# Kernel optimization log

Measured on AMD Instinct MI355X. Metric: run time of the kernel, lower is better.

## Reference

```python
import jax, jax.numpy as jnp
import numpy as np

NUM_ORI = 8      # num_orientations
P = 7            # pooled height/width (out_size)
S = 2            # num_samples (sampling grid per bin side)
SCALE = 0.25     # spatial_scale
CLOCKWISE = False


def setup_inputs() -> dict:
    key = jax.random.key(0)
    kf, kb, kc, ks, ka = jax.random.split(key, 5)
    B, C, H, W = 2, 256, 256, 256   # C = 32 channel groups x 8 orientations
    R = 512
    features = jax.random.normal(kf, (B, C, H, W), dtype=jnp.float32)
    img = H / SCALE                 # image-space extent (1024)
    batch_idx = jax.random.randint(kb, (R,), 0, B).astype(jnp.float32)
    ctr = jax.random.uniform(kc, (R, 2), minval=0.0, maxval=img)
    wh = jax.random.uniform(ks, (R, 2), minval=32.0, maxval=img * 0.25)
    ang = jax.random.uniform(ka, (R,), minval=-np.pi, maxval=np.pi)
    rois = jnp.concatenate([batch_idx[:, None], ctr, wh, ang[:, None]], axis=1)
    return {"features": features, "rois": rois}


def _riroi_align_rotated(features, rois):
    B, C, H, W = features.shape
    O = NUM_ORI
    Cg = C // O
    R = rois.shape[0]
    f32 = features.dtype

    b = rois[:, 0].astype(jnp.int32)
    cx = rois[:, 1] * SCALE
    cy = rois[:, 2] * SCALE
    rw = jnp.maximum(rois[:, 3] * SCALE, 1.0)
    rh = jnp.maximum(rois[:, 4] * SCALE, 1.0)
    theta = rois[:, 5]

    # --- orientation channel alignment (uses original-sign theta) ---
    ind_f = theta * O / (2.0 * np.pi)
    ind_floor = jnp.floor(ind_f)
    l_var = ind_f - ind_floor                         # (R,)
    r_var = 1.0 - l_var
    ind = jnp.mod(ind_floor.astype(jnp.int32), O)     # start channel, (R,)
    o = jnp.arange(O)
    ind_rot = jnp.mod(o[None, :] - ind[:, None], O)   # (R,O)
    ind_rot_p = jnp.mod(ind_rot + 1, O)

    if CLOCKWISE:
        theta = -theta

    # --- rotated sampling grid, (R, Ph, Pw, Sy, Sx) ---
    bin_h = rh / P
    bin_w = rw / P
    pidx = jnp.arange(P, dtype=f32)
    sidx = jnp.arange(S, dtype=f32)
    yy = (-rh[:, None, None] / 2.0 + pidx[None, :, None] * bin_h[:, None, None]
          + (sidx[None, None, :] + 0.5) * bin_h[:, None, None] / S)   # (R,Ph,Sy)
    xx = (-rw[:, None, None] / 2.0 + pidx[None, :, None] * bin_w[:, None, None]
          + (sidx[None, None, :] + 0.5) * bin_w[:, None, None] / S)   # (R,Pw,Sx)
    ct = jnp.cos(theta)[:, None, None, None, None]
    st = jnp.sin(theta)[:, None, None, None, None]
    X = xx[:, None, :, None, :]   # (R,1,Pw,1,Sx)
    Y = yy[:, :, None, :, None]   # (R,Ph,1,Sy,1)
    x = (X * ct - Y * st + cx[:, None, None, None, None]).reshape(R, -1)  # (R,K)
    y = (X * st + Y * ct + cy[:, None, None, None, None]).reshape(R, -1)

    # --- bilinear interpolation (matches mmcv bilinear_interpolate) ---
    valid = ~((y < -1.0) | (y > H) | (x < -1.0) | (x > W))
    yc = jnp.clip(y, 0.0, None)
    xc = jnp.clip(x, 0.0, None)
    y0 = yc.astype(jnp.int32)
    x0 = xc.astype(jnp.int32)
    hi_y = y0 >= H - 1
    hi_x = x0 >= W - 1
    y1 = jnp.where(hi_y, H - 1, y0 + 1)
    y0 = jnp.where(hi_y, H - 1, y0)
    yc = jnp.where(hi_y, y0.astype(f32), yc)
    x1 = jnp.where(hi_x, W - 1, x0 + 1)
    x0 = jnp.where(hi_x, W - 1, x0)
    xc = jnp.where(hi_x, x0.astype(f32), xc)
    ly = yc - y0.astype(f32); hy = 1.0 - ly
    lx = xc - x0.astype(f32); hx = 1.0 - lx
    vf = valid.astype(f32)
    w1 = (hy * hx * vf)[..., None]
    w2 = (hy * lx * vf)[..., None]
    w3 = (ly * hx * vf)[..., None]
    w4 = (ly * lx * vf)[..., None]

    bb = b[:, None]                                     # (R,1) -> broadcast (R,K)
    v = (w1 * features[bb, :, y0, x0] + w2 * features[bb, :, y0, x1]
         + w3 * features[bb, :, y1, x0] + w4 * features[bb, :, y1, x1])  # (R,K,C)

    # average over the SxS sample grid per bin
    v = v.reshape(R, P, P, S, S, Cg, O).mean(axis=(3, 4))   # (R,P,P,Cg,O)

    # orientation channel cyclic blend
    idx = ind_rot[:, None, None, None, :]               # (R,1,1,1,O)
    idx_p = ind_rot_p[:, None, None, None, :]
    rb = r_var[:, None, None, None, None]
    lb = l_var[:, None, None, None, None]
    out = rb * jnp.take_along_axis(v, idx, axis=4) + lb * jnp.take_along_axis(v, idx_p, axis=4)
    # (R,Ph,Pw,Cg,O) -> (R, Cg, O, Ph, Pw) -> (R, C, Ph, Pw)
    return out.transpose(0, 3, 4, 1, 2).reshape(R, Cg * O, P, P)


def reference(features, rois):
    return _riroi_align_rotated(features, rois)
```

## Files before the change

kernel.cpp:

```cpp
#include <hip/hip_runtime.h>


#define NORI 8
#define PBIN 7
#define NSAMP 2
#define CCH 256
#define HH 256
#define WW 256
#define PTOT (HH * WW)

__global__ __launch_bounds__(256) void nchw_to_nhwc_kernel(
    const float* __restrict__ feat, float* __restrict__ nhwc)
{
    __shared__ float tile[16][260];
    const int t  = threadIdx.x;
    const int b  = blockIdx.x / (PTOT / 16);
    const int p0 = (blockIdx.x % (PTOT / 16)) * 16;

    const int pl4 = (t & 3) * 4;
    const int cl  = t >> 2;
    #pragma unroll
    for (int k = 0; k < 4; ++k) {
        const int c = cl + 64 * k;
        const float4 v = *reinterpret_cast<const float4*>(
            feat + ((size_t)b * CCH + c) * PTOT + p0 + pl4);
        tile[pl4 + 0][c] = v.x;
        tile[pl4 + 1][c] = v.y;
        tile[pl4 + 2][c] = v.z;
        tile[pl4 + 3][c] = v.w;
    }
    __syncthreads();

    const int c4 = (t & 63) * 4;
    const int plb = t >> 6;
    #pragma unroll
    for (int k = 0; k < 4; ++k) {
        const int pl = plb + 4 * k;
        float4 v;
        v.x = tile[pl][c4 + 0];
        v.y = tile[pl][c4 + 1];
        v.z = tile[pl][c4 + 2];
        v.w = tile[pl][c4 + 3];
        *reinterpret_cast<float4*>(
            nhwc + ((size_t)b * PTOT + p0 + pl) * CCH + c4) = v;
    }
}

__global__ __launch_bounds__(256) void riroi_gather_nhwc_kernel(
    const float* __restrict__ nhwc,
    const float* __restrict__ rois,
    float* __restrict__ out)
{
    __shared__ float stage[64 * 49];

    const int r  = blockIdx.x >> 2;
    const int q  = blockIdx.x & 3;
    const int t  = threadIdx.x;
    const int cl = t & 63;
    const int c  = q * 64 + cl;
    const int o  = c & (NORI - 1);
    const int pix_base = t >> 6;

    const float* roi = rois + r * 6;
    const int   b     = (int)roi[0];
    const float cx    = roi[1] * 0.25f;
    const float cy    = roi[2] * 0.25f;
    const float rw    = fmaxf(roi[3] * 0.25f, 1.0f);
    const float rh    = fmaxf(roi[4] * 0.25f, 1.0f);
    const float theta = roi[5];

    const float ind_f     = theta * (8.0f / 6.283185307179586f);
    const float ind_floor = floorf(ind_f);
    const float l_var     = ind_f - ind_floor;
    const float r_var     = 1.0f - l_var;
    const int   ind       = (((int)ind_floor % NORI) + NORI) % NORI;

    const float bin_h = rh * (1.0f / (float)PBIN);
    const float bin_w = rw * (1.0f / (float)PBIN);
    const float ct = cosf(theta);
    const float st = sinf(theta);
    const float Hf = (float)HH, Wf = (float)WW;

    const float* __restrict__ fb = nhwc + (size_t)b * PTOT * CCH;

    const int lane = t & 63;
    const int lbase = lane & ~(NORI - 1);
    const int osrc  = (o - ind + NORI) & (NORI - 1);
    const int osrc1 = (osrc + 1) & (NORI - 1);

    for (int pix = pix_base; pix < PBIN * PBIN; pix += 4) {
        const int ph = pix / PBIN;
        const int pw = pix - ph * PBIN;
        const float y_base = -rh * 0.5f + (float)ph * bin_h;
        const float x_base = -rw * 0.5f + (float)pw * bin_w;

        float acc = 0.0f;
        #pragma unroll
        for (int sy = 0; sy < NSAMP; ++sy) {
            #pragma unroll
            for (int sx = 0; sx < NSAMP; ++sx) {
                const float Y = y_base + ((float)sy + 0.5f) * bin_h * 0.5f;
                const float X = x_base + ((float)sx + 0.5f) * bin_w * 0.5f;
                const float x = X * ct - Y * st + cx;
                const float y = X * st + Y * ct + cy;

                const bool valid = !((y < -1.0f) || (y > Hf) || (x < -1.0f) || (x > Wf));
                float yc = fmaxf(y, 0.0f);
                float xc = fmaxf(x, 0.0f);
                int y0 = (int)yc;
                int x0 = (int)xc;
                int y1, x1;
                if (y0 >= HH - 1) { y0 = HH - 1; y1 = HH - 1; yc = (float)y0; }
                else              { y1 = y0 + 1; }
                if (x0 >= WW - 1) { x0 = WW - 1; x1 = WW - 1; xc = (float)x0; }
                else              { x1 = x0 + 1; }

                const float ly = yc - (float)y0, hy = 1.0f - ly;
                const float lx = xc - (float)x0, hx = 1.0f - lx;
                const float vf = valid ? 1.0f : 0.0f;
                const float w1 = hy * hx * vf;
                const float w2 = hy * lx * vf;
                const float w3 = ly * hx * vf;
                const float w4 = ly * lx * vf;

                const float f00 = fb[((size_t)y0 * WW + x0) * CCH + c];
                const float f01 = fb[((size_t)y0 * WW + x1) * CCH + c];
                const float f10 = fb[((size_t)y1 * WW + x0) * CCH + c];
                const float f11 = fb[((size_t)y1 * WW + x1) * CCH + c];
                acc += w1 * f00 + w2 * f01 + w3 * f10 + w4 * f11;
            }
        }
        const float v = acc * 0.25f;

        const float v0 = __shfl(v, lbase | osrc,  64);
        const float v1 = __shfl(v, lbase | osrc1, 64);
        stage[cl * 49 + pix] = r_var * v0 + l_var * v1;
    }
    __syncthreads();

    float* __restrict__ dst = out + (size_t)r * (CCH * PBIN * PBIN) + q * (64 * PBIN * PBIN);
    #pragma unroll
    for (int k = 0; k < 13; ++k) {
        const int i = t + 256 * k;
        if (i < 64 * 49) dst[i] = stage[i];
    }
}

__global__ __launch_bounds__(256) void riroi_align_rotated_kernel(
    const float* __restrict__ feat, const float* __restrict__ rois,
    float* __restrict__ out, int C, int H, int W)
{
    const int blk = blockIdx.x;
    const int r   = blk / (PBIN * PBIN);
    const int pix = blk % (PBIN * PBIN);
    const int ph  = pix / PBIN;
    const int pw  = pix % PBIN;
    const int c   = threadIdx.x;
    const int o   = c & (NORI - 1);

    const float* roi = rois + r * 6;
    const int   b     = (int)roi[0];
    const float cx    = roi[1] * 0.25f;
    const float cy    = roi[2] * 0.25f;
    const float rw    = fmaxf(roi[3] * 0.25f, 1.0f);
    const float rh    = fmaxf(roi[4] * 0.25f, 1.0f);
    const float theta = roi[5];

    const float ind_f     = theta * (8.0f / 6.283185307179586f);
    const float ind_floor = floorf(ind_f);
    const float l_var     = ind_f - ind_floor;
    const float r_var     = 1.0f - l_var;
    const int ind = (((int)ind_floor % NORI) + NORI) % NORI;

    const float bin_h = rw * 0.0f + rh * (1.0f / (float)PBIN);
    const float bin_w = rw * (1.0f / (float)PBIN);
    const float ct = cosf(theta);
    const float st = sinf(theta);

    const float* __restrict__ fbc = feat + ((size_t)b * C + c) * (size_t)(H * W);
    const float Hf = (float)H, Wf = (float)W;
    const float y_base = -rh * 0.5f + (float)ph * bin_h;
    const float x_base = -rw * 0.5f + (float)pw * bin_w;

    float acc = 0.0f;
    #pragma unroll
    for (int sy = 0; sy < NSAMP; ++sy) {
        #pragma unroll
        for (int sx = 0; sx < NSAMP; ++sx) {
            const float Y = y_base + ((float)sy + 0.5f) * bin_h * 0.5f;
            const float X = x_base + ((float)sx + 0.5f) * bin_w * 0.5f;
            float x = X * ct - Y * st + cx;
            float y = X * st + Y * ct + cy;
            const bool valid = !((y < -1.0f) || (y > Hf) || (x < -1.0f) || (x > Wf));
            float yc = fmaxf(y, 0.0f);
            float xc = fmaxf(x, 0.0f);
            int y0 = (int)yc;
            int x0 = (int)xc;
            int y1, x1;
            if (y0 >= H - 1) { y0 = H - 1; y1 = H - 1; yc = (float)y0; }
            else             { y1 = y0 + 1; }
            if (x0 >= W - 1) { x0 = W - 1; x1 = W - 1; xc = (float)x0; }
            else             { x1 = x0 + 1; }
            const float ly = yc - (float)y0, hy = 1.0f - ly;
            const float lx = xc - (float)x0, hx = 1.0f - lx;
            const float vf = valid ? 1.0f : 0.0f;
            const float w1 = hy * hx * vf, w2 = hy * lx * vf;
            const float w3 = ly * hx * vf, w4 = ly * lx * vf;
            acc += w1 * fbc[y0 * W + x0] + w2 * fbc[y0 * W + x1]
                 + w3 * fbc[y1 * W + x0] + w4 * fbc[y1 * W + x1];
        }
    }
    const float v = acc * 0.25f;
    const int lane  = threadIdx.x & 63;
    const int base  = lane & ~(NORI - 1);
    const int osrc  = (o - ind + NORI) & (NORI - 1);
    const float v0 = __shfl(v, base | osrc, 64);
    const float v1 = __shfl(v, base | ((osrc + 1) & (NORI - 1)), 64);
    out[((size_t)r * C + c) * (PBIN * PBIN) + ph * PBIN + pw] = r_var * v0 + l_var * v1;
}

extern "C" void kernel_launch(void* const* d_in, const int* in_sizes, int n_in,
                              void* d_out, int out_size, void* d_ws, size_t ws_size,
                              hipStream_t stream) {
    const float* feat = (const float*)d_in[0];
    const float* rois = (const float*)d_in[1];
    float* out = (float*)d_out;

    const int R = in_sizes[1] / 6;
    const int B = in_sizes[0] / (CCH * PTOT);
    const size_t need = (size_t)B * PTOT * CCH * sizeof(float);

    if (ws_size >= need) {
        float* nhwc = (float*)d_ws;
        nchw_to_nhwc_kernel<<<dim3(B * (PTOT / 16)), dim3(256), 0, stream>>>(feat, nhwc);
        riroi_gather_nhwc_kernel<<<dim3(R * 4), dim3(256), 0, stream>>>(nhwc, rois, out);
    } else {
        riroi_align_rotated_kernel<<<dim3(R * PBIN * PBIN), dim3(256), 0, stream>>>(
            feat, rois, out, CCH, HH, WW);
    }
}
```

Measured before the change: 279.2 us.

## Retile NHWC transpose and vectorize gather with float4 channel loads

The transpose kernel now handles 32 pixels by 128 channels per block and issues all global loads before the shared-memory writes, which gives more loads in flight. The gather kernel has each thread load four adjacent channels with float4 reads and process four pixels in an unrolled loop. The orientation blend moves from wavefront shuffles to the shared-memory write-back stage, where it costs extra LDS reads and integer index math. This trades fewer, wider memory transactions and more memory parallelism against more per-thread registers and possible LDS bank conflicts.

```diff
diff --git a/kernel.cpp b/kernel.cpp
--- a/kernel.cpp
+++ b/kernel.cpp
@@ -3,7 +3,7 @@
 
 #define NORI 8
 #define PBIN 7
-#define NSAMP 2
+#define NPIX 49
 #define CCH 256
 #define HH 256
 #define WW 256
@@ -12,37 +12,48 @@
 __global__ __launch_bounds__(256) void nchw_to_nhwc_kernel(
     const float* __restrict__ feat, float* __restrict__ nhwc)
 {
-    __shared__ float tile[16][260];
-    const int t  = threadIdx.x;
-    const int b  = blockIdx.x / (PTOT / 16);
-    const int p0 = (blockIdx.x % (PTOT / 16)) * 16;
-
-    const int pl4 = (t & 3) * 4;
-    const int cl  = t >> 2;
-    #pragma unroll
-    for (int k = 0; k < 4; ++k) {
-        const int c = cl + 64 * k;
-        const float4 v = *reinterpret_cast<const float4*>(
-            feat + ((size_t)b * CCH + c) * PTOT + p0 + pl4);
-        tile[pl4 + 0][c] = v.x;
-        tile[pl4 + 1][c] = v.y;
-        tile[pl4 + 2][c] = v.z;
-        tile[pl4 + 3][c] = v.w;
+    __shared__ float tile[32 * 132];
+    const int t = threadIdx.x;
+    int blk = blockIdx.x;
+    const int b    = blk >> 12;
+    blk &= 4095;
+    const int c0   = (blk & 1) * 128;
+    const int p0   = (blk >> 1) * 32;
+
+    const float* __restrict__ src = feat + ((size_t)b * CCH + c0) * PTOT + p0;
+
+    float4 v[4];
+    #pragma unroll
+    for (int k = 0; k < 4; ++k) {
+        const int flat = t + 256 * k;
+        const int c    = flat >> 3;
+        const int p4   = (flat & 7) * 4;
+        v[k] = *reinterpret_cast<const float4*>(src + (size_t)c * PTOT + p4);
+    }
+    #pragma unroll
+    for (int k = 0; k < 4; ++k) {
+        const int flat = t + 256 * k;
+        const int c    = flat >> 3;
+        const int p4   = (flat & 7) * 4;
+        tile[(p4 + 0) * 132 + c] = v[k].x;
+        tile[(p4 + 1) * 132 + c] = v[k].y;
+        tile[(p4 + 2) * 132 + c] = v[k].z;
+        tile[(p4 + 3) * 132 + c] = v[k].w;
     }
     __syncthreads();
 
-    const int c4 = (t & 63) * 4;
-    const int plb = t >> 6;
-    #pragma unroll
-    for (int k = 0; k < 4; ++k) {
-        const int pl = plb + 4 * k;
-        float4 v;
-        v.x = tile[pl][c4 + 0];
-        v.y = tile[pl][c4 + 1];
-        v.z = tile[pl][c4 + 2];
-        v.w = tile[pl][c4 + 3];
-        *reinterpret_cast<float4*>(
-            nhwc + ((size_t)b * PTOT + p0 + pl) * CCH + c4) = v;
+    float* __restrict__ dst = nhwc + ((size_t)b * PTOT + p0) * CCH + c0;
+    #pragma unroll
+    for (int k = 0; k < 4; ++k) {
+        const int flat = t + 256 * k;
+        const int p    = flat >> 5;
+        const int cg4  = (flat & 31) * 4;
+        float4 w;
+        w.x = tile[p * 132 + cg4 + 0];
+        w.y = tile[p * 132 + cg4 + 1];
+        w.z = tile[p * 132 + cg4 + 2];
+        w.w = tile[p * 132 + cg4 + 3];
+        *reinterpret_cast<float4*>(dst + (size_t)p * CCH + cg4) = w;
     }
 }
 
@@ -51,15 +62,14 @@
     const float* __restrict__ rois,
     float* __restrict__ out)
 {
-    __shared__ float stage[64 * 49];
-
-    const int r  = blockIdx.x >> 2;
-    const int q  = blockIdx.x & 3;
-    const int t  = threadIdx.x;
-    const int cl = t & 63;
-    const int c  = q * 64 + cl;
-    const int o  = c & (NORI - 1);
-    const int pix_base = t >> 6;
+    __shared__ float stage[64 * NPIX];
+
+    const int r   = blockIdx.x >> 2;
+    const int q   = blockIdx.x & 3;
+    const int t   = threadIdx.x;
+    const int cl4 = (t & 15) * 4;
+    const int c4  = q * 64 + cl4;
+    const int pixlane = t >> 4;
 
     const float* roi = rois + r * 6;
     const int   b     = (int)roi[0];
@@ -83,66 +93,79 @@
 
     const float* __restrict__ fb = nhwc + (size_t)b * PTOT * CCH;
 
-    const int lane = t & 63;
-    const int lbase = lane & ~(NORI - 1);
-    const int osrc  = (o - ind + NORI) & (NORI - 1);
-    const int osrc1 = (osrc + 1) & (NORI - 1);
-
-    for (int pix = pix_base; pix < PBIN * PBIN; pix += 4) {
-        const int ph = pix / PBIN;
-        const int pw = pix - ph * PBIN;
-        const float y_base = -rh * 0.5f + (float)ph * bin_h;
-        const float x_base = -rw * 0.5f + (float)pw * bin_w;
-
-        float acc = 0.0f;
-        #pragma unroll
-        for (int sy = 0; sy < NSAMP; ++sy) {
+    #pragma unroll
+    for (int k = 0; k < 4; ++k) {
+        const int pix = pixlane + 16 * k;
+        if (pix < NPIX) {
+            const int ph = pix / PBIN;
+            const int pw = pix - ph * PBIN;
+            const float y_base = -rh * 0.5f + (float)ph * bin_h;
+            const float x_base = -rw * 0.5f + (float)pw * bin_w;
+
+            float ax = 0.0f, ay = 0.0f, az = 0.0f, aw = 0.0f;
             #pragma unroll
-            for (int sx = 0; sx < NSAMP; ++sx) {
-                const float Y = y_base + ((float)sy + 0.5f) * bin_h * 0.5f;
-                const float X = x_base + ((float)sx + 0.5f) * bin_w * 0.5f;
-                const float x = X * ct - Y * st + cx;
-                const float y = X * st + Y * ct + cy;
-
-                const bool valid = !((y < -1.0f) || (y > Hf) || (x < -1.0f) || (x > Wf));
-                float yc = fmaxf(y, 0.0f);
-                float xc = fmaxf(x, 0.0f);
-                int y0 = (int)yc;
-                int x0 = (int)xc;
-                int y1, x1;
-                if (y0 >= HH - 1) { y0 = HH - 1; y1 = HH - 1; yc = (float)y0; }
-                else              { y1 = y0 + 1; }
-                if (x0 >= WW - 1) { x0 = WW - 1; x1 = WW - 1; xc = (float)x0; }
-                else              { x1 = x0 + 1; }
-
-                const float ly = yc - (float)y0, hy = 1.0f - ly;
-                const float lx = xc - (float)x0, hx = 1.0f - lx;
-                const float vf = valid ? 1.0f : 0.0f;
-                const float w1 = hy * hx * vf;
-                const float w2 = hy * lx * vf;
-                const float w3 = ly * hx * vf;
-                const float w4 = ly * lx * vf;
-
-                const float f00 = fb[((size_t)y0 * WW + x0) * CCH + c];
-                const float f01 = fb[((size_t)y0 * WW + x1) * CCH + c];
-                const float f10 = fb[((size_t)y1 * WW + x0) * CCH + c];
-                const float f11 = fb[((size_t)y1 * WW + x1) * CCH + c];
-                acc += w1 * f00 + w2 * f01 + w3 * f10 + w4 * f11;
+            for (int sy = 0; sy < 2; ++sy) {
+                #pragma unroll
+                for (int sx = 0; sx < 2; ++sx) {
+                    const float Y = y_base + ((float)sy + 0.5f) * bin_h * 0.5f;
+                    const float X = x_base + ((float)sx + 0.5f) * bin_w * 0.5f;
+                    const float x = X * ct - Y * st + cx;
+                    const float y = X * st + Y * ct + cy;
+
+                    const bool valid = !((y < -1.0f) || (y > Hf) || (x < -1.0f) || (x > Wf));
+                    float yc = fmaxf(y, 0.0f);
+                    float xc = fmaxf(x, 0.0f);
+                    int y0 = (int)yc;
+                    int x0 = (int)xc;
+                    int y1, x1;
+                    if (y0 >= HH - 1) { y0 = HH - 1; y1 = HH - 1; yc = (float)y0; }
+                    else              { y1 = y0 + 1; }
+                    if (x0 >= WW - 1) { x0 = WW - 1; x1 = WW - 1; xc = (float)x0; }
+                    else              { x1 = x0 + 1; }
+
+                    const float ly = yc - (float)y0, hy = 1.0f - ly;
+                    const float lx = xc - (float)x0, hx = 1.0f - lx;
+                    const float vf = valid ? 1.0f : 0.0f;
+                    const float w1 = hy * hx * vf;
+                    const float w2 = hy * lx * vf;
+                    const float w3 = ly * hx * vf;
+                    const float w4 = ly * lx * vf;
+
+                    const float4 f00 = *reinterpret_cast<const float4*>(
+                        fb + ((size_t)(y0 * WW + x0)) * CCH + c4);
+                    const float4 f01 = *reinterpret_cast<const float4*>(
+                        fb + ((size_t)(y0 * WW + x1)) * CCH + c4);
+                    const float4 f10 = *reinterpret_cast<const float4*>(
+                        fb + ((size_t)(y1 * WW + x0)) * CCH + c4);
+                    const float4 f11 = *reinterpret_cast<const float4*>(
+                        fb + ((size_t)(y1 * WW + x1)) * CCH + c4);
+
+                    ax += w1 * f00.x + w2 * f01.x + w3 * f10.x + w4 * f11.x;
+                    ay += w1 * f00.y + w2 * f01.y + w3 * f10.y + w4 * f11.y;
+                    az += w1 * f00.z + w2 * f01.z + w3 * f10.z + w4 * f11.z;
+                    aw += w1 * f00.w + w2 * f01.w + w3 * f10.w + w4 * f11.w;
+                }
             }
+            stage[(cl4 + 0) * NPIX + pix] = ax * 0.25f;
+            stage[(cl4 + 1) * NPIX + pix] = ay * 0.25f;
+            stage[(cl4 + 2) * NPIX + pix] = az * 0.25f;
+            stage[(cl4 + 3) * NPIX + pix] = aw * 0.25f;
         }
-        const float v = acc * 0.25f;
-
-        const float v0 = __shfl(v, lbase | osrc,  64);
-        const float v1 = __shfl(v, lbase | osrc1, 64);
-        stage[cl * 49 + pix] = r_var * v0 + l_var * v1;
     }
     __syncthreads();
 
-    float* __restrict__ dst = out + (size_t)r * (CCH * PBIN * PBIN) + q * (64 * PBIN * PBIN);
+    float* __restrict__ dst = out + (size_t)r * (CCH * NPIX) + q * (64 * NPIX);
     #pragma unroll
     for (int k = 0; k < 13; ++k) {
         const int i = t + 256 * k;
-        if (i < 64 * 49) dst[i] = stage[i];
+        if (i < 64 * NPIX) {
+            const int c   = i / NPIX;
+            const int pix = i - c * NPIX;
+            const int o   = c & (NORI - 1);
+            const int s0  = (c & ~(NORI - 1)) | ((o - ind + 8) & (NORI - 1));
+            const int s1  = (c & ~(NORI - 1)) | ((o - ind + 9) & (NORI - 1));
+            dst[i] = r_var * stage[s0 * NPIX + pix] + l_var * stage[s1 * NPIX + pix];
+        }
     }
 }
 
@@ -172,7 +195,7 @@
     const float r_var     = 1.0f - l_var;
     const int ind = (((int)ind_floor % NORI) + NORI) % NORI;
 
-    const float bin_h = rw * 0.0f + rh * (1.0f / (float)PBIN);
+    const float bin_h = rh * (1.0f / (float)PBIN);
     const float bin_w = rw * (1.0f / (float)PBIN);
     const float ct = cosf(theta);
     const float st = sinf(theta);
@@ -184,9 +207,9 @@
 
     float acc = 0.0f;
     #pragma unroll
-    for (int sy = 0; sy < NSAMP; ++sy) {
+    for (int sy = 0; sy < 2; ++sy) {
         #pragma unroll
-        for (int sx = 0; sx < NSAMP; ++sx) {
+        for (int sx = 0; sx < 2; ++sx) {
             const float Y = y_base + ((float)sy + 0.5f) * bin_h * 0.5f;
             const float X = x_base + ((float)sx + 0.5f) * bin_w * 0.5f;
             float x = X * ct - Y * st + cx;
@@ -232,7 +255,7 @@
 
     if (ws_size >= need) {
         float* nhwc = (float*)d_ws;
-        nchw_to_nhwc_kernel<<<dim3(B * (PTOT / 16)), dim3(256), 0, stream>>>(feat, nhwc);
+        nchw_to_nhwc_kernel<<<dim3(B * 4096), dim3(256), 0, stream>>>(feat, nhwc);
         riroi_gather_nhwc_kernel<<<dim3(R * 4), dim3(256), 0, stream>>>(nhwc, rois, out);
     } else {
         riroi_align_rotated_kernel<<<dim3(R * PBIN * PBIN), dim3(256), 0, stream>>>(
```

Result: faster. 269.8 us (-3.4%).
